# Kernel optimization log

Measured on AMD Instinct MI355X. Metric: run time of the kernel, lower is better.

The kernel has to match this reference:

```python
import jax, jax.numpy as jnp
import numpy as np

T, H, P = 8192, 512, 512
DT_MIN, DT_MAX = 0.001, 0.1
STEP_RESCALE = 1.0


def setup_inputs() -> dict:
    key = jax.random.key(0)
    ks = jax.random.split(key, 8)
    x = jax.random.normal(ks[0], (T, H), dtype=jnp.float32)
    # sparse reset flags (episode boundaries)
    mask = jax.random.bernoulli(ks[1], 0.005, (T,)).astype(jnp.float32)
    carry = jnp.zeros((1, P, 2), dtype=jnp.float32)  # initial complex state as (re, im)
    # HiPPO-DPLR-style eigenvalue init: lambda_k = -0.5 + i*pi*k
    lambda_real = -0.5 * jnp.ones((P,), dtype=jnp.float32)
    lambda_imag = jnp.pi * jnp.arange(P, dtype=jnp.float32)
    b = jax.random.normal(ks[2], (P, H, 2), dtype=jnp.float32) / np.sqrt(H)
    c = jax.random.normal(ks[3], (H, P, 2), dtype=jnp.float32) * np.sqrt(0.5)
    d = jax.random.normal(ks[4], (H,), dtype=jnp.float32)
    u = jax.random.uniform(ks[5], (P, 1), dtype=jnp.float32)
    log_step = np.log(DT_MIN) + u * (np.log(DT_MAX) - np.log(DT_MIN))
    return {"x": x, "mask": mask, "carry": carry, "lambda_real": lambda_real,
            "lambda_imag": lambda_imag, "b": b, "c": c, "d": d, "log_step": log_step}


def _binary_operator_reset(q_i, q_j):
    a_i, b_i, c_i = q_i
    a_j, b_j, c_j = q_j
    a_out = a_j * a_i * (1.0 - c_j) + a_j * c_j
    b_out = (a_j * b_i + b_j) * (1.0 - c_j) + b_j * c_j
    c_out = c_i * (1.0 - c_j) + c_j
    return (a_out, b_out, c_out)


def reference(x, mask, carry, lambda_real, lambda_imag, b, c, d, log_step):
    t = x.shape[0]
    # clip_eigens=True: force stability
    lam_re = jnp.minimum(lambda_real, -0.0001)
    lam = jax.lax.complex(lam_re, lambda_imag).astype(jnp.complex64)  # [P]
    b_tilde = jax.lax.complex(b[..., 0], b[..., 1]).astype(jnp.complex64)  # [P,H]
    c_tilde = jax.lax.complex(c[..., 0], c[..., 1]).astype(jnp.complex64)  # [H,P]
    step = (STEP_RESCALE * jnp.exp(log_step[:, 0].astype(jnp.float32))).astype(jnp.complex64)  # [P]
    # ZOH discretization
    lambda_bar = jnp.exp(lam * step)                      # [P]
    b_bar = ((lambda_bar - 1.0) / lam)[:, None] * b_tilde  # [P,H]
    # scan elements
    a = jnp.broadcast_to(lambda_bar, (t, P))
    a = jnp.concatenate([jnp.ones((1, P), dtype=lambda_bar.dtype), a])  # [T+1,P]
    b_x = x.astype(jnp.complex64) @ b_bar.T                              # [T,P]
    carry0 = jax.lax.complex(carry[..., 0], carry[..., 1]).astype(jnp.complex64)  # [1,P]
    b_x = jnp.concatenate([carry0, b_x])                                 # [T+1,P]
    m = jnp.concatenate([jnp.zeros((1,), x.dtype), mask])[:, None]       # [T+1,1]
    _, states, _ = jax.lax.associative_scan(_binary_operator_reset, (a, b_x, m))
    states = states[1:]                                                  # [T,P] complex
    ys = jnp.real(states @ c_tilde.T) + d * x                            # [T,H]
    final_carry = states[-1][None]                                       # [1,P] complex
    return (final_carry, ys)
```

## Files before the change

kernel.cpp:

```cpp
#include <hip/hip_runtime.h>
#include <hip/hip_bf16.h>

#define T_LEN 8192
#define H_DIM 512
#define P_DIM 512
#define CS 32
#define NB (T_LEN / CS)

typedef __attribute__((ext_vector_type(8))) __bf16 bf16x8;
typedef __attribute__((ext_vector_type(4))) float f32x4;

__device__ __forceinline__ unsigned short f2bf(float f) {
    __bf16 h = (__bf16)f;
    return __builtin_bit_cast(unsigned short, h);
}
__device__ __forceinline__ float bf2f(unsigned short u) {
    unsigned v = ((unsigned)u) << 16;
    return __builtin_bit_cast(float, v);
}

__device__ __forceinline__ void gload_lds16(void* g, void* l) {
    __builtin_amdgcn_global_load_lds(
        (__attribute__((address_space(1))) unsigned*)g,
        (__attribute__((address_space(3))) unsigned*)l, 16, 0, 0);
}

__global__ __launch_bounds__(512) void precompute_p1(
    const float* __restrict__ lambda_real,
    const float* __restrict__ lambda_imag,
    const float* __restrict__ log_step,
    double* __restrict__ lbar,
    double* __restrict__ coef) {
    int p = threadIdx.x;
    double lr = fmin((double)lambda_real[p], -1e-4);
    double li = (double)lambda_imag[p];
    double step = exp((double)log_step[p]);
    double er = exp(lr * step);
    double ang = li * step;
    double lbr = er * cos(ang);
    double lbi = er * sin(ang);
    lbar[2 * p] = lbr;
    lbar[2 * p + 1] = lbi;
    double nr = lbr - 1.0, ni = lbi;
    double den = lr * lr + li * li;
    coef[2 * p]     = (nr * lr + ni * li) / den;
    coef[2 * p + 1] = (ni * lr - nr * li) / den;
}

__global__ __launch_bounds__(256) void prep_kernel(
    const float* __restrict__ x,
    const float* __restrict__ b, const float* __restrict__ c,
    const double* __restrict__ coef,
    unsigned short* __restrict__ xhi, unsigned short* __restrict__ xlo,
    unsigned short* __restrict__ Bt1hi, unsigned short* __restrict__ Bt1lo,
    unsigned short* __restrict__ Bt2hi, unsigned short* __restrict__ Bt2lo) {
    int idx = blockIdx.x * 256 + threadIdx.x;
    {
        float4 v = ((const float4*)x)[idx];
        ushort4 h, l;
        h.x = f2bf(v.x); l.x = f2bf(v.x - bf2f(h.x));
        h.y = f2bf(v.y); l.y = f2bf(v.y - bf2f(h.y));
        h.z = f2bf(v.z); l.z = f2bf(v.z - bf2f(h.z));
        h.w = f2bf(v.w); l.w = f2bf(v.w - bf2f(h.w));
        ((ushort4*)xhi)[idx] = h;
        ((ushort4*)xlo)[idx] = l;
    }
    if (blockIdx.x < (P_DIM * H_DIM) / 256) {
        int idx2 = blockIdx.x * 256 + threadIdx.x;
        {
            int p = idx2 >> 9, h = idx2 & 511;
            double cr = coef[2 * p], ci = coef[2 * p + 1];
            float2 bv = ((const float2*)b)[(size_t)p * H_DIM + h];
            float re = (float)(cr * (double)bv.x - ci * (double)bv.y);
            float im = (float)(cr * (double)bv.y + ci * (double)bv.x);
            unsigned short rh = f2bf(re), ih = f2bf(im);
            Bt1hi[(size_t)(2 * p) * H_DIM + h]     = rh;
            Bt1lo[(size_t)(2 * p) * H_DIM + h]     = f2bf(re - bf2f(rh));
            Bt1hi[(size_t)(2 * p + 1) * H_DIM + h] = ih;
            Bt1lo[(size_t)(2 * p + 1) * H_DIM + h] = f2bf(im - bf2f(ih));
        }
        {
            int h = idx2 >> 9, p = idx2 & 511;
            float2 cv = ((const float2*)c)[(size_t)h * P_DIM + p];
            float re = cv.x, im = -cv.y;
            ushort2 hi, lo;
            hi.x = f2bf(re); lo.x = f2bf(re - bf2f(hi.x));
            hi.y = f2bf(im); lo.y = f2bf(im - bf2f(hi.y));
            ((ushort2*)Bt2hi)[(size_t)h * P_DIM + p] = hi;
            ((ushort2*)Bt2lo)[(size_t)h * P_DIM + p] = lo;
        }
    }
}

template <int MODE>
__global__ __launch_bounds__(256) void gemm_mfma_split(
    const unsigned short* __restrict__ Ahi, const unsigned short* __restrict__ Alo,
    int lda,
    const unsigned short* __restrict__ Bthi, const unsigned short* __restrict__ Btlo,
    int ldb,
    void* __restrict__ Cout0, void* __restrict__ Cout1, int ldc, int K,
    const float* __restrict__ Dvec, const float* __restrict__ X) {
    __shared__ __align__(16) unsigned short lds[2][4][128 * 32];
    const int tid = threadIdx.x;
    const int lane = tid & 63, wid = tid >> 6;
    const int wm = wid >> 1, wn = wid & 1;

    const int id = blockIdx.y * gridDim.x + blockIdx.x;
    const int nx = gridDim.x, rpx = gridDim.y >> 3;
    const int xcd = id & 7, j = id >> 3;
    const int by = xcd * rpx + j / nx;
    const int bx = j % nx;
    const int bm = by * 128, bn = bx * 128;

    const unsigned short* ssrc;
    int srow0, sld;
    if (wid == 0)      { ssrc = Ahi;  srow0 = bm; sld = lda; }
    else if (wid == 1) { ssrc = Alo;  srow0 = bm; sld = lda; }
    else if (wid == 2) { ssrc = Bthi; srow0 = bn; sld = ldb; }
    else               { ssrc = Btlo; srow0 = bn; sld = ldb; }

    f32x4 acc[4][4];
#pragma unroll
    for (int i = 0; i < 4; ++i)
#pragma unroll
        for (int j2 = 0; j2 < 4; ++j2) acc[i][j2] = (f32x4)(0.0f);

    auto stage = [&](int buf, int k0) {
        unsigned short* base = &lds[buf][wid][0];
#pragma unroll
        for (int s = 0; s < 8; ++s) {
            int r = s * 16 + (lane >> 2);
            int cg = (lane & 3) ^ ((r >> 1) & 3);
            void* g = (void*)((const char*)(ssrc + (size_t)(srow0 + r) * sld + k0)
                              + cg * 16);
            gload_lds16(g, (void*)((char*)base + s * 1024));
        }
    };

    stage(0, 0);
    __syncthreads();

    const int nk = K / 32;
    for (int t = 0; t < nk; ++t) {
        int cur = t & 1;
        if (t + 1 < nk) stage(cur ^ 1, (t + 1) * 32);

        bf16x8 ah[4], al[4], bh[4], bl[4];
#pragma unroll
        for (int i = 0; i < 4; ++i) {
            int rA = wm * 64 + i * 16 + (lane & 15);
            int byA = rA * 64 + ((((lane >> 4)) ^ ((rA >> 1) & 3)) << 4);
            ah[i] = *(const bf16x8*)((const char*)&lds[cur][0][0] + byA);
            al[i] = *(const bf16x8*)((const char*)&lds[cur][1][0] + byA);
            int rB = wn * 64 + i * 16 + (lane & 15);
            int byB = rB * 64 + ((((lane >> 4)) ^ ((rB >> 1) & 3)) << 4);
            bh[i] = *(const bf16x8*)((const char*)&lds[cur][2][0] + byB);
            bl[i] = *(const bf16x8*)((const char*)&lds[cur][3][0] + byB);
        }
#pragma unroll
        for (int i = 0; i < 4; ++i)
#pragma unroll
            for (int j2 = 0; j2 < 4; ++j2) {
                acc[i][j2] = __builtin_amdgcn_mfma_f32_16x16x32_bf16(
                    ah[i], bh[j2], acc[i][j2], 0, 0, 0);
                acc[i][j2] = __builtin_amdgcn_mfma_f32_16x16x32_bf16(
                    ah[i], bl[j2], acc[i][j2], 0, 0, 0);
                acc[i][j2] = __builtin_amdgcn_mfma_f32_16x16x32_bf16(
                    al[i], bh[j2], acc[i][j2], 0, 0, 0);
            }
        __syncthreads();
    }

#pragma unroll
    for (int i = 0; i < 4; ++i)
#pragma unroll
        for (int j2 = 0; j2 < 4; ++j2) {
            int col = bn + wn * 64 + j2 * 16 + (lane & 15);
#pragma unroll
            for (int r = 0; r < 4; ++r) {
                int row = bm + wm * 64 + i * 16 + (lane >> 4) * 4 + r;
                float v = acc[i][j2][r];
                if (MODE == 0) {
                    unsigned short h = f2bf(v);
                    unsigned short lo = f2bf(v - bf2f(h));
                    ((unsigned short*)Cout0)[(size_t)row * ldc + col] = h;
                    ((unsigned short*)Cout1)[(size_t)row * ldc + col] = lo;
                } else {
                    v += Dvec[col] * X[(size_t)row * ldc + col];
                    ((float*)Cout0)[(size_t)row * ldc + col] = v;
                }
            }
        }
}

__global__ __launch_bounds__(512) void scanA_kernel(
    const unsigned short* __restrict__ Shi, const unsigned short* __restrict__ Slo,
    const float* __restrict__ mask, const double* __restrict__ lbar,
    double* __restrict__ cA, double* __restrict__ cS, float* __restrict__ cC) {
    int p = threadIdx.x;
    int blk = blockIdx.x;
    double lbr = lbar[2 * p], lbi = lbar[2 * p + 1];
    double Ar = 1., Ai = 0., Sr = 0., Si = 0.;
    float C = 0.f;
    const ushort2* H2 = (const ushort2*)Shi;
    const ushort2* L2 = (const ushort2*)Slo;
    int t0 = blk * CS;
    for (int t = t0; t < t0 + CS; ++t) {
        float m = mask[t];
        ushort2 h2 = H2[(size_t)t * P_DIM + p];
        ushort2 l2 = L2[(size_t)t * P_DIM + p];
        double bxr = (double)(bf2f(h2.x) + bf2f(l2.x));
        double bxi = (double)(bf2f(h2.y) + bf2f(l2.y));
        if (m != 0.f) {
            Ar = lbr; Ai = lbi; Sr = bxr; Si = bxi; C = 1.f;
        } else {
            double nAr = lbr * Ar - lbi * Ai;
            Ai = lbr * Ai + lbi * Ar; Ar = nAr;
            double nSr = lbr * Sr - lbi * Si + bxr;
            Si = lbr * Si + lbi * Sr + bxi; Sr = nSr;
        }
    }
    cA[(size_t)blk * 1024 + 2 * p] = Ar;
    cA[(size_t)blk * 1024 + 2 * p + 1] = Ai;
    cS[(size_t)blk * 1024 + 2 * p] = Sr;
    cS[(size_t)blk * 1024 + 2 * p + 1] = Si;
    cC[(size_t)blk * P_DIM + p] = C;
}

__global__ __launch_bounds__(256) void scanB_kernel(
    const double* __restrict__ cA, const double* __restrict__ cS,
    const float* __restrict__ cC, const float* __restrict__ carry,
    double* __restrict__ prefix) {
    int p = blockIdx.x;
    int i = threadIdx.x;
    __shared__ double sAr[NB], sAi[NB], sSr[NB], sSi[NB];
    __shared__ float sC[NB];

    double Ar = cA[(size_t)i * 1024 + 2 * p];
    double Ai = cA[(size_t)i * 1024 + 2 * p + 1];
    double Sr = cS[(size_t)i * 1024 + 2 * p];
    double Si = cS[(size_t)i * 1024 + 2 * p + 1];
    float  C  = cC[(size_t)i * P_DIM + p];
    sAr[i] = Ar; sAi[i] = Ai; sSr[i] = Sr; sSi[i] = Si; sC[i] = C;
    __syncthreads();

    for (int step = 1; step < NB; step <<= 1) {
        double pAr = 0, pAi = 0, pSr = 0, pSi = 0; float pC = 0;
        if (i >= step) {
            pAr = sAr[i - step]; pAi = sAi[i - step];
            pSr = sSr[i - step]; pSi = sSi[i - step]; pC = sC[i - step];
        }
        __syncthreads();
        if (i >= step && C == 0.f) {
            double nAr = Ar * pAr - Ai * pAi;
            double nAi = Ar * pAi + Ai * pAr;
            double nSr = Ar * pSr - Ai * pSi + Sr;
            double nSi = Ar * pSi + Ai * pSr + Si;
            Ar = nAr; Ai = nAi; Sr = nSr; Si = nSi; C = pC;
        }
        sAr[i] = Ar; sAi[i] = Ai; sSr[i] = Sr; sSi[i] = Si; sC[i] = C;
        __syncthreads();
    }

    double c0r = (double)carry[2 * p], c0i = (double)carry[2 * p + 1];
    double pr, pi_;
    if (i == 0) {
        pr = c0r; pi_ = c0i;
    } else {
        double Lr = sAr[i - 1], Li = sAi[i - 1];
        double Tr = sSr[i - 1], Ti = sSi[i - 1];
        float  LC = sC[i - 1];
        if (LC != 0.f) { pr = Tr; pi_ = Ti; }
        else {
            pr  = Lr * c0r - Li * c0i + Tr;
            pi_ = Lr * c0i + Li * c0r + Ti;
        }
    }
    prefix[(size_t)i * 1024 + 2 * p]     = pr;
    prefix[(size_t)i * 1024 + 2 * p + 1] = pi_;
}

__global__ __launch_bounds__(512) void scanC_kernel(
    unsigned short* __restrict__ Shi, unsigned short* __restrict__ Slo,
    const float* __restrict__ mask, const double* __restrict__ lbar,
    const double* __restrict__ prefix,
    float* __restrict__ carry_out, int carry_elems) {
    int p = threadIdx.x;
    int blk = blockIdx.x;
    double lbr = lbar[2 * p], lbi = lbar[2 * p + 1];
    double sr = prefix[(size_t)blk * 1024 + 2 * p];
    double si = prefix[(size_t)blk * 1024 + 2 * p + 1];
    ushort2* H2 = (ushort2*)Shi;
    ushort2* L2 = (ushort2*)Slo;
    int t0 = blk * CS;
    for (int t = t0; t < t0 + CS; ++t) {
        float m = mask[t];
        ushort2 h2 = H2[(size_t)t * P_DIM + p];
        ushort2 l2 = L2[(size_t)t * P_DIM + p];
        double bxr = (double)(bf2f(h2.x) + bf2f(l2.x));
        double bxi = (double)(bf2f(h2.y) + bf2f(l2.y));
        if (m != 0.f) {
            sr = bxr; si = bxi;
        } else {
            double nr = lbr * sr - lbi * si + bxr;
            si = lbr * si + lbi * sr + bxi;
            sr = nr;
        }
        float sf = (float)sr, sif = (float)si;
        ushort2 ho, lo;
        ho.x = f2bf(sf);  lo.x = f2bf(sf - bf2f(ho.x));
        ho.y = f2bf(sif); lo.y = f2bf(sif - bf2f(ho.y));
        H2[(size_t)t * P_DIM + p] = ho;
        L2[(size_t)t * P_DIM + p] = lo;
    }
    if (blk == NB - 1) {
        if (carry_elems >= 1024) {
            carry_out[2 * p] = (float)sr;
            carry_out[2 * p + 1] = (float)si;
        } else {
            carry_out[p] = (float)sr;
        }
    }
}

extern "C" void kernel_launch(void* const* d_in, const int* in_sizes, int n_in,
                              void* d_out, int out_size, void* d_ws, size_t ws_size,
                              hipStream_t stream) {
    const float* x           = (const float*)d_in[0];
    const float* mask        = (const float*)d_in[1];
    const float* carry       = (const float*)d_in[2];
    const float* lambda_real = (const float*)d_in[3];
    const float* lambda_imag = (const float*)d_in[4];
    const float* b           = (const float*)d_in[5];
    const float* c           = (const float*)d_in[6];
    const float* d           = (const float*)d_in[7];
    const float* log_step    = (const float*)d_in[8];

    float* out = (float*)d_out;
    char* ws = (char*)d_ws;

    int carry_elems = out_size - T_LEN * H_DIM;
    if (carry_elems != 512 && carry_elems != 1024) carry_elems = 1024;
    float* ys_out = out + carry_elems;

    double* lbar   = (double*)ws;                        ws += 1024 * 8;
    double* coef   = (double*)ws;                        ws += 1024 * 8;
    double* cA     = (double*)ws;                        ws += (size_t)NB * 1024 * 8;
    double* cSb    = (double*)ws;                        ws += (size_t)NB * 1024 * 8;
    double* prefix = (double*)ws;                        ws += (size_t)NB * 1024 * 8;
    float* cC      = (float*)ws;                         ws += (size_t)NB * P_DIM * 4;
    unsigned short* xhi   = (unsigned short*)ws;         ws += (size_t)T_LEN * H_DIM * 2;
    unsigned short* xlo   = (unsigned short*)ws;         ws += (size_t)T_LEN * H_DIM * 2;
    unsigned short* Bt1hi = (unsigned short*)ws;         ws += (size_t)(2 * P_DIM) * H_DIM * 2;
    unsigned short* Bt1lo = (unsigned short*)ws;         ws += (size_t)(2 * P_DIM) * H_DIM * 2;
    unsigned short* Bt2hi = (unsigned short*)ws;         ws += (size_t)H_DIM * (2 * P_DIM) * 2;
    unsigned short* Bt2lo = (unsigned short*)ws;         ws += (size_t)H_DIM * (2 * P_DIM) * 2;
    unsigned short* Shi   = (unsigned short*)ws;         ws += (size_t)T_LEN * (2 * P_DIM) * 2;
    unsigned short* Slo   = (unsigned short*)ws;         ws += (size_t)T_LEN * (2 * P_DIM) * 2;

    precompute_p1<<<1, 512, 0, stream>>>(lambda_real, lambda_imag, log_step,
                                         lbar, coef);
    prep_kernel<<<(T_LEN * H_DIM / 4) / 256, 256, 0, stream>>>(
        x, b, c, coef, xhi, xlo, Bt1hi, Bt1lo, Bt2hi, Bt2lo);

    {
        dim3 grid((2 * P_DIM) / 128, T_LEN / 128);
        gemm_mfma_split<0><<<grid, 256, 0, stream>>>(
            xhi, xlo, H_DIM, Bt1hi, Bt1lo, H_DIM,
            Shi, Slo, 2 * P_DIM, H_DIM, nullptr, nullptr);
    }

    scanA_kernel<<<NB, 512, 0, stream>>>(Shi, Slo, mask, lbar, cA, cSb, cC);
    scanB_kernel<<<P_DIM, NB, 0, stream>>>(cA, cSb, cC, carry, prefix);
    scanC_kernel<<<NB, 512, 0, stream>>>(Shi, Slo, mask, lbar, prefix, out,
                                         carry_elems);

    {
        dim3 grid(H_DIM / 128, T_LEN / 128);
        gemm_mfma_split<1><<<grid, 256, 0, stream>>>(
            Shi, Slo, 2 * P_DIM, Bt2hi, Bt2lo, 2 * P_DIM,
            ys_out, nullptr, H_DIM, 2 * P_DIM, d, x);
    }
}
```

Before: 114.5 us.

## Fuse chunk-local scan reduction into first GEMM epilogue via LDS

```diff
diff --git a/kernel.cpp b/kernel.cpp
--- a/kernel.cpp
+++ b/kernel.cpp
@@ -4,7 +4,7 @@
 #define T_LEN 8192
 #define H_DIM 512
 #define P_DIM 512
-#define CS 32
+#define CS 16
 #define NB (T_LEN / CS)
 
 typedef __attribute__((ext_vector_type(8))) __bf16 bf16x8;
@@ -99,7 +99,9 @@
     const unsigned short* __restrict__ Bthi, const unsigned short* __restrict__ Btlo,
     int ldb,
     void* __restrict__ Cout0, void* __restrict__ Cout1, int ldc, int K,
-    const float* __restrict__ Dvec, const float* __restrict__ X) {
+    const float* __restrict__ Dvec, const float* __restrict__ X,
+    const float* __restrict__ mask, const double* __restrict__ lbar,
+    double* __restrict__ cA, double* __restrict__ cS, float* __restrict__ cC) {
     __shared__ __align__(16) unsigned short lds[2][4][128 * 32];
     const int tid = threadIdx.x;
     const int lane = tid & 63, wid = tid >> 6;
@@ -191,43 +193,54 @@
                 }
             }
         }
-}
-
-__global__ __launch_bounds__(512) void scanA_kernel(
-    const unsigned short* __restrict__ Shi, const unsigned short* __restrict__ Slo,
-    const float* __restrict__ mask, const double* __restrict__ lbar,
-    double* __restrict__ cA, double* __restrict__ cS, float* __restrict__ cC) {
-    int p = threadIdx.x;
-    int blk = blockIdx.x;
-    double lbr = lbar[2 * p], lbi = lbar[2 * p + 1];
-    double Ar = 1., Ai = 0., Sr = 0., Si = 0.;
-    float C = 0.f;
-    const ushort2* H2 = (const ushort2*)Shi;
-    const ushort2* L2 = (const ushort2*)Slo;
-    int t0 = blk * CS;
-    for (int t = t0; t < t0 + CS; ++t) {
-        float m = mask[t];
-        ushort2 h2 = H2[(size_t)t * P_DIM + p];
-        ushort2 l2 = L2[(size_t)t * P_DIM + p];
-        double bxr = (double)(bf2f(h2.x) + bf2f(l2.x));
-        double bxi = (double)(bf2f(h2.y) + bf2f(l2.y));
-        if (m != 0.f) {
-            Ar = lbr; Ai = lbi; Sr = bxr; Si = bxi; C = 1.f;
-        } else {
-            double nAr = lbr * Ar - lbi * Ai;
-            Ai = lbr * Ai + lbi * Ar; Ar = nAr;
-            double nSr = lbr * Sr - lbi * Si + bxr;
-            Si = lbr * Si + lbi * Sr + bxi; Sr = nSr;
-        }
-    }
-    cA[(size_t)blk * 1024 + 2 * p] = Ar;
-    cA[(size_t)blk * 1024 + 2 * p + 1] = Ai;
-    cS[(size_t)blk * 1024 + 2 * p] = Sr;
-    cS[(size_t)blk * 1024 + 2 * p + 1] = Si;
-    cC[(size_t)blk * P_DIM + p] = C;
-}
-
-__global__ __launch_bounds__(256) void scanB_kernel(
+
+    if constexpr (MODE == 0) {
+        float* fl = (float*)&lds[0][0][0];
+#pragma unroll
+        for (int i = 0; i < 4; ++i)
+#pragma unroll
+            for (int j2 = 0; j2 < 4; ++j2) {
+                int lcol = wn * 64 + j2 * 16 + (lane & 15);
+#pragma unroll
+                for (int r = 0; r < 4; ++r) {
+                    int lrow = wm * 64 + i * 16 + (lane >> 4) * 4 + r;
+                    fl[lrow * 128 + lcol] = acc[i][j2][r];
+                }
+            }
+        __syncthreads();
+        const int NCH = 128 / CS;
+        for (int w = tid; w < 64 * NCH; w += 256) {
+            int q = w & 63;
+            int ck = w >> 6;
+            int pg = (bn >> 1) + q;
+            double lbr = lbar[2 * pg], lbi = lbar[2 * pg + 1];
+            double Ar = 1., Ai = 0., Sr = 0., Si = 0.;
+            float Cc = 0.f;
+            for (int k = 0; k < CS; ++k) {
+                int row = ck * CS + k;
+                float m = mask[bm + row];
+                double bxr = (double)fl[row * 128 + 2 * q];
+                double bxi = (double)fl[row * 128 + 2 * q + 1];
+                if (m != 0.f) {
+                    Ar = lbr; Ai = lbi; Sr = bxr; Si = bxi; Cc = 1.f;
+                } else {
+                    double nAr = lbr * Ar - lbi * Ai;
+                    Ai = lbr * Ai + lbi * Ar; Ar = nAr;
+                    double nSr = lbr * Sr - lbi * Si + bxr;
+                    Si = lbr * Si + lbi * Sr + bxi; Sr = nSr;
+                }
+            }
+            int cg = (bm / CS) + ck;
+            cA[(size_t)cg * 1024 + 2 * pg]     = Ar;
+            cA[(size_t)cg * 1024 + 2 * pg + 1] = Ai;
+            cS[(size_t)cg * 1024 + 2 * pg]     = Sr;
+            cS[(size_t)cg * 1024 + 2 * pg + 1] = Si;
+            cC[(size_t)cg * P_DIM + pg] = Cc;
+        }
+    }
+}
+
+__global__ __launch_bounds__(NB) void scanB_kernel(
     const double* __restrict__ cA, const double* __restrict__ cS,
     const float* __restrict__ cC, const float* __restrict__ carry,
     double* __restrict__ prefix) {
@@ -367,10 +380,10 @@
         dim3 grid((2 * P_DIM) / 128, T_LEN / 128);
         gemm_mfma_split<0><<<grid, 256, 0, stream>>>(
             xhi, xlo, H_DIM, Bt1hi, Bt1lo, H_DIM,
-            Shi, Slo, 2 * P_DIM, H_DIM, nullptr, nullptr);
-    }
-
-    scanA_kernel<<<NB, 512, 0, stream>>>(Shi, Slo, mask, lbar, cA, cSb, cC);
+            Shi, Slo, 2 * P_DIM, H_DIM, nullptr, nullptr,
+            mask, lbar, cA, cSb, cC);
+    }
+
     scanB_kernel<<<P_DIM, NB, 0, stream>>>(cA, cSb, cC, carry, prefix);
     scanC_kernel<<<NB, 512, 0, stream>>>(Shi, Slo, mask, lbar, prefix, out,
                                          carry_elems);
@@ -379,6 +392,7 @@
         dim3 grid(H_DIM / 128, T_LEN / 128);
         gemm_mfma_split<1><<<grid, 256, 0, stream>>>(
             Shi, Slo, 2 * P_DIM, Bt2hi, Bt2lo, 2 * P_DIM,
-            ys_out, nullptr, H_DIM, 2 * P_DIM, d, x);
-    }
-}
+            ys_out, nullptr, H_DIM, 2 * P_DIM, d, x,
+            nullptr, nullptr, nullptr, nullptr, nullptr);
+    }
+}
```

Result: faster. 111.3 us (-2.8%).
